# Kernel tuning notes

Measured on AMD Instinct MI355X. Metric: run time of the kernel, lower is better.

## Reference

```python
import jax, jax.numpy as jnp
import numpy as np

HEADS = 30
HEAD_DIM = 64
DIM = HEADS * HEAD_DIM  # 1920
TXT = 226
VID = 2048
EPS = 1e-5


def setup_inputs() -> dict:
    key = jax.random.key(0)
    ks = jax.random.split(key, 12)
    s = 1.0 / np.sqrt(DIM)
    return {
        "hidden_states": jax.random.normal(ks[0], (1, VID, DIM), jnp.float32),
        "encoder_hidden_states": jax.random.normal(ks[1], (1, TXT, DIM), jnp.float32),
        "rope_cos": jax.random.uniform(ks[2], (VID, HEAD_DIM), jnp.float32, -1.0, 1.0),
        "rope_sin": jax.random.uniform(ks[3], (VID, HEAD_DIM), jnp.float32, -1.0, 1.0),
        "Wq": jax.random.normal(ks[4], (DIM, DIM), jnp.float32) * s,
        "bq": jnp.zeros((DIM,), jnp.float32),
        "Wk": jax.random.normal(ks[5], (DIM, DIM), jnp.float32) * s,
        "bk": jnp.zeros((DIM,), jnp.float32),
        "Wv": jax.random.normal(ks[6], (DIM, DIM), jnp.float32) * s,
        "bv": jnp.zeros((DIM,), jnp.float32),
        "ln_q_w": jnp.ones((HEAD_DIM,), jnp.float32),
        "ln_q_b": jnp.zeros((HEAD_DIM,), jnp.float32),
        "ln_k_w": jnp.ones((HEAD_DIM,), jnp.float32),
        "ln_k_b": jnp.zeros((HEAD_DIM,), jnp.float32),
        "Wo": jax.random.normal(ks[7], (DIM, DIM), jnp.float32) * s,
        "bo": jnp.zeros((DIM,), jnp.float32),
    }


def _layernorm(x, w, b):
    mu = jnp.mean(x, axis=-1, keepdims=True)
    var = jnp.var(x, axis=-1, keepdims=True)
    return (x - mu) * jax.lax.rsqrt(var + EPS) * w + b


def _apply_rope(x, cos, sin):
    # x: [B,H,S_vid,D]; cos/sin: [S_vid,D]. Interleaved-pair rotation (diffusers use_real, unbind_dim=-1).
    xr = x[..., 0::2]
    xi = x[..., 1::2]
    rot = jnp.stack([-xi, xr], axis=-1).reshape(x.shape)
    return x * cos + rot * sin


def reference(hidden_states, encoder_hidden_states, rope_cos, rope_sin,
              Wq, bq, Wk, bk, Wv, bv, ln_q_w, ln_q_b, ln_k_w, ln_k_b, Wo, bo):
    T = encoder_hidden_states.shape[1]
    h = jnp.concatenate([encoder_hidden_states, hidden_states], axis=1)  # [B,S,D]
    B, S, _ = h.shape

    def proj(W, bias):
        y = h @ W.T + bias
        return y.reshape(B, S, HEADS, HEAD_DIM).transpose(0, 2, 1, 3)  # [B,H,S,d]

    q = proj(Wq, bq)
    k = proj(Wk, bk)
    v = proj(Wv, bv)

    q = _layernorm(q, ln_q_w, ln_q_b)
    k = _layernorm(k, ln_k_w, ln_k_b)

    # rotary embedding applied only to the image/video tokens
    q = jnp.concatenate([q[:, :, :T], _apply_rope(q[:, :, T:], rope_cos, rope_sin)], axis=2)
    k = jnp.concatenate([k[:, :, :T], _apply_rope(k[:, :, T:], rope_cos, rope_sin)], axis=2)

    scale = 1.0 / np.sqrt(HEAD_DIM)
    scores = jnp.einsum("bhqd,bhkd->bhqk", q, k) * scale
    attn = jax.nn.softmax(scores, axis=-1)
    out = jnp.einsum("bhqk,bhkd->bhqd", attn, v)

    out = out.transpose(0, 2, 1, 3).reshape(B, S, DIM)
    out = out @ Wo.T + bo
    return out[:, T:], out[:, :T]
```

## Files before the change

kernel.cpp:

```cpp
#include <hip/hip_runtime.h>
#include <hip/hip_bf16.h>

typedef __hip_bfloat16 bf16;
using f32x4 = __attribute__((ext_vector_type(4))) float;
using f32x16 = __attribute__((ext_vector_type(16))) float;
using s16x8 = __attribute__((ext_vector_type(8))) short;

#define S_TOT 2274
#define S_PAD 2304
#define TTXT 226
#define DIMN 1920
#define NH 30
#define HD 64
#define NQKV 5760
#define QSCALE 0.1803368801f

#define GLOAD_LDS16(g, l)                                                              \
  __builtin_amdgcn_global_load_lds((const __attribute__((address_space(1))) void*)(g), \
                                   (__attribute__((address_space(3))) void*)(l), 16, 0, 0)

__global__ void k_prep_h(const float* __restrict__ hid, const float* __restrict__ enc,
                         bf16* __restrict__ h_bf) {
  long i4 = ((long)blockIdx.x * blockDim.x + threadIdx.x) * 4;
  if (i4 >= (long)S_PAD * DIMN) return;
  int s = (int)(i4 / DIMN);
  float4 v = make_float4(0.f, 0.f, 0.f, 0.f);
  if (s < TTXT)
    v = *reinterpret_cast<const float4*>(enc + i4);
  else if (s < S_TOT)
    v = *reinterpret_cast<const float4*>(hid + i4 - (long)TTXT * DIMN);
  union {
    bf16 b[4];
    short4 s4;
  } o;
  o.b[0] = __float2bfloat16(v.x);
  o.b[1] = __float2bfloat16(v.y);
  o.b[2] = __float2bfloat16(v.z);
  o.b[3] = __float2bfloat16(v.w);
  *reinterpret_cast<short4*>(h_bf + i4) = o.s4;
}

__global__ void k_prep_wqkv(const float* __restrict__ Wq, const float* __restrict__ Wk,
                            const float* __restrict__ Wv, bf16* __restrict__ w_bf) {
  long i4 = ((long)blockIdx.x * blockDim.x + threadIdx.x) * 4;
  const long per = (long)DIMN * DIMN;
  if (i4 >= 3 * per) return;
  const float* src = (i4 < per) ? (Wq + i4) : (i4 < 2 * per) ? (Wk + i4 - per) : (Wv + i4 - 2 * per);
  float4 v = *reinterpret_cast<const float4*>(src);
  union {
    bf16 b[4];
    short4 s4;
  } o;
  o.b[0] = __float2bfloat16(v.x);
  o.b[1] = __float2bfloat16(v.y);
  o.b[2] = __float2bfloat16(v.z);
  o.b[3] = __float2bfloat16(v.w);
  *reinterpret_cast<short4*>(w_bf + i4) = o.s4;
}

__global__ void k_prep_wo(const float* __restrict__ Wo, bf16* __restrict__ w_bf) {
  long i4 = ((long)blockIdx.x * blockDim.x + threadIdx.x) * 4;
  if (i4 >= (long)DIMN * DIMN) return;
  float4 v = *reinterpret_cast<const float4*>(Wo + i4);
  union {
    bf16 b[4];
    short4 s4;
  } o;
  o.b[0] = __float2bfloat16(v.x);
  o.b[1] = __float2bfloat16(v.y);
  o.b[2] = __float2bfloat16(v.z);
  o.b[3] = __float2bfloat16(v.w);
  *reinterpret_cast<short4*>(w_bf + i4) = o.s4;
}

#define NKT 30
#define BUFSZ 49152
__global__ __launch_bounds__(512, 2) void k_gemm_qkv8(
    const bf16* __restrict__ A, const bf16* __restrict__ B, const float* __restrict__ bq,
    const float* __restrict__ bk, const float* __restrict__ bv, const float* __restrict__ lqw,
    const float* __restrict__ lqb, const float* __restrict__ lkw, const float* __restrict__ lkb,
    const float* __restrict__ cosT, const float* __restrict__ sinT, bf16* __restrict__ qb,
    bf16* __restrict__ kbf, bf16* __restrict__ vt) {
  __shared__ __align__(16) char smem[3 * BUFSZ];
  const int tid = threadIdx.x;
  const int w = tid >> 6, lane = tid & 63;
  const int clo = lane & 15, lhi = lane >> 4;
  const int wr = w >> 1, wc = w & 1;
  const int m0 = blockIdx.y * 256, n0 = blockIdx.x * 128;

  long ga[4], gb[2];
#pragma unroll
  for (int i = 0; i < 4; ++i) {
    const int s = i * 512 + tid;
    const int row = s >> 3, gch = (s & 7) ^ ((s >> 3) & 7);
    ga[i] = (long)(m0 + row) * DIMN + gch * 8;
  }
#pragma unroll
  for (int i = 0; i < 2; ++i) {
    const int s = i * 512 + tid;
    const int row = s >> 3, gch = (s & 7) ^ ((s >> 3) & 7);
    gb[i] = (long)(n0 + row) * DIMN + gch * 8;
  }
  const int wbase = w * 1024;

  auto stage = [&](int b, int kt) {
    char* Ab = &smem[b * BUFSZ];
    char* Bb = Ab + 32768;
    const int ko = kt * 64;
#pragma unroll
    for (int i = 0; i < 4; ++i) GLOAD_LDS16(A + ga[i] + ko, Ab + i * 8192 + wbase);
#pragma unroll
    for (int i = 0; i < 2; ++i) GLOAD_LDS16(B + gb[i] + ko, Bb + i * 8192 + wbase);
  };

  auto rdf = [&](const char* base, int row, int slot) {
    return *reinterpret_cast<const s16x8*>(base + row * 128 + ((slot ^ (row & 7)) * 16));
  };

  f32x4 acc[4][4] = {};

  stage(0, 0);
  stage(1, 1);
  for (int t = 0; t < NKT; ++t) {
    if (t < NKT - 1)
      asm volatile("s_waitcnt vmcnt(6)" ::: "memory");
    else
      asm volatile("s_waitcnt vmcnt(0)" ::: "memory");
    __builtin_amdgcn_s_barrier();
    if (t + 2 < NKT) stage((t + 2) % 3, t + 2);
    const char* Ab = &smem[(t % 3) * BUFSZ];
    const char* Bb = Ab + 32768;
#pragma unroll
    for (int ks = 0; ks < 2; ++ks) {
      s16x8 af[4], bfr[4];
#pragma unroll
      for (int m = 0; m < 4; ++m) af[m] = rdf(Ab, wr * 64 + m * 16 + clo, ks * 4 + lhi);
#pragma unroll
      for (int n = 0; n < 4; ++n) bfr[n] = rdf(Bb, wc * 64 + n * 16 + clo, ks * 4 + lhi);
      __builtin_amdgcn_s_setprio(1);
#pragma unroll
      for (int m = 0; m < 4; ++m)
#pragma unroll
        for (int n = 0; n < 4; ++n)
          acc[m][n] = __builtin_amdgcn_mfma_f32_16x16x32_bf16(af[m], bfr[n], acc[m][n], 0, 0, 0);
      __builtin_amdgcn_s_setprio(0);
    }
  }
  __syncthreads();

  const int gcol0 = n0 + wc * 64;
  const int sect = gcol0 / DIMN;
  const int hcol = gcol0 - sect * DIMN;
  const int head = hcol >> 6;
  const int row0 = m0 + wr * 64;

  if (sect < 2) {
    const float* bias = sect ? bk : bq;
    const float* lw = sect ? lkw : lqw;
    const float* lb = sect ? lkb : lqb;
    bf16* dst = sect ? kbf : qb;
    const float oscale = sect ? 1.f : QSCALE;
    float bb[4], lww[4], lbb[4];
#pragma unroll
    for (int n = 0; n < 4; ++n) {
      const int d = (n << 4) + clo;
      bb[n] = bias[hcol + d];
      lww[n] = lw[d];
      lbb[n] = lb[d];
    }
#pragma unroll
    for (int m = 0; m < 4; ++m) {
#pragma unroll
      for (int r = 0; r < 4; ++r) {
        const int row = row0 + m * 16 + lhi * 4 + r;
        float x[4];
#pragma unroll
        for (int n = 0; n < 4; ++n) x[n] = acc[m][n][r] + bb[n];
        float s_ = (x[0] + x[1]) + (x[2] + x[3]);
        float q_ = x[0] * x[0];
        q_ = fmaf(x[1], x[1], q_);
        q_ = fmaf(x[2], x[2], q_);
        q_ = fmaf(x[3], x[3], q_);
#pragma unroll
        for (int off = 1; off <= 8; off <<= 1) {
          s_ += __shfl_xor(s_, off);
          q_ += __shfl_xor(q_, off);
        }
        const float mu = s_ * (1.f / 64.f);
        const float var = q_ * (1.f / 64.f) - mu * mu;
        const float rst = rsqrtf(var + 1e-5f);
        float xn[4];
#pragma unroll
        for (int n = 0; n < 4; ++n) xn[n] = (x[n] - mu) * rst * lww[n] + lbb[n];
        const bool dorope = (row >= TTXT) && (row < S_TOT);
        if (dorope) {
          const float* cr = cosT + (long)(row - TTXT) * HD;
          const float* sr2 = sinT + (long)(row - TTXT) * HD;
#pragma unroll
          for (int n = 0; n < 4; ++n) {
            const int d = (n << 4) + clo;
            const float p = __shfl_xor(xn[n], 1);
            xn[n] = xn[n] * cr[d] + ((clo & 1) ? p : -p) * sr2[d];
          }
        }
#pragma unroll
        for (int n = 0; n < 4; ++n)
          dst[((long)head * S_PAD + row) * HD + (n << 4) + clo] =
              __float2bfloat16(xn[n] * oscale);
      }
    }
  } else {
    float bb[4];
#pragma unroll
    for (int n = 0; n < 4; ++n) bb[n] = bv[hcol + (n << 4) + clo];
    bf16* Lp = reinterpret_cast<bf16*>(smem + w * 9216);
#pragma unroll
    for (int m = 0; m < 4; ++m)
#pragma unroll
      for (int n = 0; n < 4; ++n)
#pragma unroll
        for (int r = 0; r < 4; ++r)
          Lp[((n << 4) + clo) * 72 + m * 16 + lhi * 4 + r] =
              __float2bfloat16(acc[m][n][r] + bb[n]);
    const int dsub = lane >> 3, sc = lane & 7;
#pragma unroll
    for (int it = 0; it < 8; ++it) {
      const int d = it * 8 + dsub;
      s16x8 v = *reinterpret_cast<const s16x8*>(&Lp[d * 72 + sc * 8]);
      *reinterpret_cast<s16x8*>(vt + ((long)head * HD + d) * S_PAD + row0 + sc * 8) = v;
    }
  }
}

__global__ __launch_bounds__(256) void k_gemm_proj(const bf16* __restrict__ A,
                                                   const bf16* __restrict__ B,
                                                   float* __restrict__ C,
                                                   const float* __restrict__ bias) {
  __shared__ __align__(16) char smem[32768];
  const int tid = threadIdx.x;
  const int w = tid >> 6, lane = tid & 63;
  const int clo = lane & 15, lhi = lane >> 4;
  const int wr = w >> 1, wc = w & 1;
  const int m0 = blockIdx.y * 128, n0 = blockIdx.x * 128;

  const int srow = tid >> 2, schunk = tid & 3;
  const long agoff0 = (long)(m0 + srow) * DIMN + schunk * 8;
  const long agoff1 = agoff0 + (long)64 * DIMN;
  const long bgoff0 = (long)(n0 + srow) * DIMN + schunk * 8;
  const long bgoff1 = bgoff0 + (long)64 * DIMN;
  const int ldsb = w * 1024;

  f32x4 acc[4][4] = {};

  auto stage = [&](int b, int kb) {
    char* Abuf = &smem[b * 16384];
    char* Bbuf = &smem[b * 16384 + 8192];
    GLOAD_LDS16(A + agoff0 + kb, Abuf + ldsb);
    GLOAD_LDS16(A + agoff1 + kb, Abuf + 4096 + ldsb);
    GLOAD_LDS16(B + bgoff0 + kb, Bbuf + ldsb);
    GLOAD_LDS16(B + bgoff1 + kb, Bbuf + 4096 + ldsb);
  };

  stage(0, 0);
  __syncthreads();
  int cur = 0;
  for (int ks = 0; ks < DIMN / 32; ++ks) {
    if (ks + 1 < DIMN / 32) stage(cur ^ 1, (ks + 1) * 32);
    const char* Abuf = &smem[cur * 16384];
    const char* Bbuf = &smem[cur * 16384 + 8192];
    s16x8 af[4], bfr[4];
#pragma unroll
    for (int m = 0; m < 4; ++m)
      af[m] = *reinterpret_cast<const s16x8*>(Abuf + (wr * 64 + m * 16 + clo) * 64 + lhi * 16);
#pragma unroll
    for (int n = 0; n < 4; ++n)
      bfr[n] = *reinterpret_cast<const s16x8*>(Bbuf + (wc * 64 + n * 16 + clo) * 64 + lhi * 16);
#pragma unroll
    for (int m = 0; m < 4; ++m)
#pragma unroll
      for (int n = 0; n < 4; ++n)
        acc[m][n] = __builtin_amdgcn_mfma_f32_16x16x32_bf16(af[m], bfr[n], acc[m][n], 0, 0, 0);
    __syncthreads();
    cur ^= 1;
  }
#pragma unroll
  for (int n = 0; n < 4; ++n) {
    const int col = n0 + wc * 64 + n * 16 + clo;
    const float bvv = bias[col];
#pragma unroll
    for (int m = 0; m < 4; ++m) {
#pragma unroll
      for (int r = 0; r < 4; ++r) {
        const int row = m0 + wr * 64 + m * 16 + lhi * 4 + r;
        if (row < S_TOT) {
          const int dst = (row >= TTXT) ? (row - TTXT) : (row + (S_TOT - TTXT));
          C[(long)dst * DIMN + col] = acc[m][n][r] + bvv;
        }
      }
    }
  }
}

__global__ __launch_bounds__(256) void k_flash6(const bf16* __restrict__ qb,
                                                const bf16* __restrict__ kbf,
                                                const bf16* __restrict__ vt,
                                                float* __restrict__ po,
                                                float* __restrict__ pm,
                                                float* __restrict__ pl) {
  __shared__ __align__(16) char smem[32768];
  const int h = blockIdx.x, qt = blockIdx.y, ks = blockIdx.z;
  const int tid = threadIdx.x, w = tid >> 6, lane = tid & 63;
  const int l31 = lane & 31, hf = lane >> 5;
  const bf16* Qh = qb + (long)h * S_PAD * HD;
  const bf16* Kh = kbf + (long)h * S_PAD * HD;
  const bf16* Vh = vt + (long)h * HD * S_PAD;
  const int q0w = qt * 128 + w * 32;
  const int T0 = ks * 18;

  s16x8 qf[4];
#pragma unroll
  for (int t = 0; t < 4; ++t)
    qf[t] = *reinterpret_cast<const s16x8*>(Qh + (long)(q0w + l31) * HD + t * 16 + hf * 8);

  f32x16 accO[2] = {};
  f32x16 lacc = {};
  float m_run = -1e30f;

  const s16x8 ones8 = {0x3F80, 0x3F80, 0x3F80, 0x3F80, 0x3F80, 0x3F80, 0x3F80, 0x3F80};

  const int su = w * 64 + lane;
  const int sr = su >> 3, sc8 = su & 7;
  const long kg0 = (long)sr * HD + ((sc8 ^ (sr & 7)) * 8);
  const long kg1 = kg0 + (long)32 * HD;
  const long vg0 = (long)sr * S_PAD + ((sc8 ^ (sr & 7)) * 8);
  const long vg1 = vg0 + (long)32 * S_PAD;
  const int ldsb = w * 1024;

  auto stage = [&](int b, int kb0) {
    char* Kb = &smem[b * 16384];
    char* Vb = &smem[b * 16384 + 8192];
    GLOAD_LDS16(Kh + (long)kb0 * HD + kg0, Kb + ldsb);
    GLOAD_LDS16(Kh + (long)kb0 * HD + kg1, Kb + 4096 + ldsb);
    GLOAD_LDS16(Vh + kb0 + vg0, Vb + ldsb);
    GLOAD_LDS16(Vh + kb0 + vg1, Vb + 4096 + ldsb);
  };

  auto ldsrd = [&](const char* base, int row, int c) {
    return *reinterpret_cast<const s16x8*>(base + row * 128 + ((c ^ (row & 7)) * 16));
  };
  auto pk2 = [&](float a, float b) -> unsigned {
    __hip_bfloat162 t = __float22bfloat162_rn(make_float2(a, b));
    return *reinterpret_cast<unsigned*>(&t);
  };

  stage(0, T0 * 64);
  __syncthreads();
  int cur = 0;
  for (int kt = 0; kt < 18; ++kt) {
    const int kb0 = (T0 + kt) * 64;
    if (kt + 1 < 18) stage(cur ^ 1, kb0 + 64);
    const char* Kb = &smem[cur * 16384];
    const char* Vb = &smem[cur * 16384 + 8192];

    f32x16 s0 = {}, s1 = {};
#pragma unroll
    for (int t = 0; t < 4; ++t) {
      s16x8 k0 = ldsrd(Kb, l31, 2 * t + hf);
      s16x8 k1 = ldsrd(Kb, 32 + l31, 2 * t + hf);
      s0 = __builtin_amdgcn_mfma_f32_32x32x16_bf16(k0, qf[t], s0, 0, 0, 0);
      s1 = __builtin_amdgcn_mfma_f32_32x32x16_bf16(k1, qf[t], s1, 0, 0, 0);
    }
    if (kb0 + 64 > S_TOT) {
#pragma unroll
      for (int j = 0; j < 16; ++j) {
        const int key = kb0 + (j & 3) + 8 * (j >> 2) + 4 * hf;
        if (key >= S_TOT) s0[j] = -1e30f;
        if (key + 32 >= S_TOT) s1[j] = -1e30f;
      }
    }
    float a8[8];
#pragma unroll
    for (int i = 0; i < 8; ++i)
      a8[i] = fmaxf(fmaxf(s0[2 * i], s0[2 * i + 1]), fmaxf(s1[2 * i], s1[2 * i + 1]));
    float pmax = fmaxf(fmaxf(fmaxf(a8[0], a8[1]), fmaxf(a8[2], a8[3])),
                       fmaxf(fmaxf(a8[4], a8[5]), fmaxf(a8[6], a8[7])));
    {
      auto r = __builtin_amdgcn_permlane32_swap(__float_as_uint(pmax), __float_as_uint(pmax),
                                                false, false);
      pmax = fmaxf(__uint_as_float(r[0]), __uint_as_float(r[1]));
    }
    if (!__all(pmax - m_run <= 8.f)) {
      const float mnew = fmaxf(m_run, pmax);
      const float corr = exp2f(m_run - mnew);
      m_run = mnew;
#pragma unroll
      for (int j = 0; j < 16; ++j) {
        const float cj = __shfl(corr, (lane & 32) | ((j & 3) + 8 * (j >> 2) + 4 * hf));
        accO[0][j] *= cj;
        accO[1][j] *= cj;
        lacc[j] *= cj;
      }
    }
#pragma unroll
    for (int j = 0; j < 16; ++j) {
      s0[j] = exp2f(s0[j] - m_run);
      s1[j] = exp2f(s1[j] - m_run);
    }
    unsigned gw0[8], gw1[8];
#pragma unroll
    for (int i = 0; i < 4; ++i) {
      gw0[2 * i] = pk2(s0[4 * i], s0[4 * i + 1]);
      gw0[2 * i + 1] = pk2(s0[4 * i + 2], s0[4 * i + 3]);
      gw1[2 * i] = pk2(s1[4 * i], s1[4 * i + 1]);
      gw1[2 * i + 1] = pk2(s1[4 * i + 2], s1[4 * i + 3]);
    }
    s16x8 pa[4];
#pragma unroll
    for (int b = 0; b < 2; ++b) {
      unsigned* gw = b ? gw1 : gw0;
#pragma unroll
      for (int t = 0; t < 2; ++t) {
        auto rA = __builtin_amdgcn_permlane32_swap(gw[4 * t + 0], gw[4 * t + 2], false, false);
        auto rB = __builtin_amdgcn_permlane32_swap(gw[4 * t + 1], gw[4 * t + 3], false, false);
        union {
          unsigned u[4];
          s16x8 v;
        } A;
        A.u[0] = rA[0];
        A.u[1] = rB[0];
        A.u[2] = rA[1];
        A.u[3] = rB[1];
        pa[b * 2 + t] = A.v;
      }
    }
#pragma unroll
    for (int t4 = 0; t4 < 4; ++t4) {
      s16x8 v0 = ldsrd(Vb, l31, 2 * t4 + hf);
      s16x8 v1 = ldsrd(Vb, 32 + l31, 2 * t4 + hf);
      accO[0] = __builtin_amdgcn_mfma_f32_32x32x16_bf16(pa[t4], v0, accO[0], 0, 0, 0);
      accO[1] = __builtin_amdgcn_mfma_f32_32x32x16_bf16(pa[t4], v1, accO[1], 0, 0, 0);
      lacc = __builtin_amdgcn_mfma_f32_32x32x16_bf16(pa[t4], ones8, lacc, 0, 0, 0);
    }
    __syncthreads();
    cur ^= 1;
  }
  const long rowbase = ((long)(ks * NH + h)) * S_PAD + q0w;
  if (hf == 0) pm[rowbase + l31] = m_run;
  if (l31 == 0) {
#pragma unroll
    for (int j = 0; j < 16; ++j) pl[rowbase + (j & 3) + 8 * (j >> 2) + 4 * hf] = lacc[j];
  }
#pragma unroll
  for (int j = 0; j < 16; ++j) {
    const int pat = (j & 3) + 8 * (j >> 2) + 4 * hf;
    float* dst = po + (rowbase + pat) * HD + l31;
    dst[0] = accO[0][j];
    dst[32] = accO[1][j];
  }
}

__global__ __launch_bounds__(256) void k_combine(const float* __restrict__ po,
                                                 const float* __restrict__ pm,
                                                 const float* __restrict__ pl,
                                                 bf16* __restrict__ ao) {
  const int idx = blockIdx.x * 256 + threadIdx.x;
  const int d = idx & 63;
  const int row = (idx >> 6) % S_PAD;
  const int h = idx / (S_PAD * 64);
  if (row >= S_TOT) return;
  const long r1 = (long)h * S_PAD + row;
  const long r2 = (long)(NH + h) * S_PAD + row;
  const float m1 = pm[r1], m2 = pm[r2];
  const float m = fmaxf(m1, m2);
  const float a1 = exp2f(m1 - m), a2 = exp2f(m2 - m);
  const float o = po[r1 * HD + d] * a1 + po[r2 * HD + d] * a2;
  const float l = pl[r1] * a1 + pl[r2] * a2;
  ao[(long)row * DIMN + h * HD + d] = __float2bfloat16(o / l);
}

extern "C" void kernel_launch(void* const* d_in, const int* in_sizes, int n_in, void* d_out,
                              int out_size, void* d_ws, size_t ws_size, hipStream_t stream) {
  const float* hid = (const float*)d_in[0];
  const float* enc = (const float*)d_in[1];
  const float* rc = (const float*)d_in[2];
  const float* rs = (const float*)d_in[3];
  const float* Wq = (const float*)d_in[4];
  const float* bq = (const float*)d_in[5];
  const float* Wk = (const float*)d_in[6];
  const float* bk = (const float*)d_in[7];
  const float* Wv = (const float*)d_in[8];
  const float* bv = (const float*)d_in[9];
  const float* lqw = (const float*)d_in[10];
  const float* lqb = (const float*)d_in[11];
  const float* lkw = (const float*)d_in[12];
  const float* lkb = (const float*)d_in[13];
  const float* Wo = (const float*)d_in[14];
  const float* bo = (const float*)d_in[15];
  float* out = (float*)d_out;

  char* ws = (char*)d_ws;
  size_t off = 0;
  char* scratch = ws + off;
  off += (size_t)S_PAD * NQKV * 4;
  bf16* h_bf = (bf16*)(ws + off);
  off += (size_t)S_PAD * DIMN * 2;
  bf16* wqkv = (bf16*)(ws + off);
  off += (size_t)3 * DIMN * DIMN * 2;
  bf16* wo = (bf16*)(ws + off);
  off += (size_t)DIMN * DIMN * 2;
  bf16* q_bf = (bf16*)(ws + off);
  off += (size_t)NH * S_PAD * HD * 2;
  bf16* k_bf = (bf16*)(ws + off);
  off += (size_t)NH * S_PAD * HD * 2;
  bf16* vt_bf = (bf16*)(ws + off);
  off += (size_t)NH * HD * S_PAD * 2;
  bf16* at_bf = (bf16*)(ws + off);
  off += (size_t)S_PAD * DIMN * 2;

  float* po = (float*)scratch;
  float* pm = (float*)(scratch + (size_t)2 * NH * S_PAD * HD * 4);
  float* pl = pm + (size_t)2 * NH * S_PAD;

  k_prep_h<<<((S_PAD * DIMN) / 4 + 255) / 256, 256, 0, stream>>>(hid, enc, h_bf);
  k_prep_wqkv<<<((3 * DIMN * DIMN) / 4 + 255) / 256, 256, 0, stream>>>(Wq, Wk, Wv, wqkv);
  k_prep_wo<<<((DIMN * DIMN) / 4 + 255) / 256, 256, 0, stream>>>(Wo, wo);
  k_gemm_qkv8<<<dim3(NQKV / 128, S_PAD / 256), 512, 0, stream>>>(
      h_bf, wqkv, bq, bk, bv, lqw, lqb, lkw, lkb, rc, rs, q_bf, k_bf, vt_bf);
  k_flash6<<<dim3(NH, S_PAD / 128, 2), 256, 0, stream>>>(q_bf, k_bf, vt_bf, po, pm, pl);
  k_combine<<<NH * S_PAD * HD / 256, 256, 0, stream>>>(po, pm, pl, at_bf);
  k_gemm_proj<<<dim3(DIMN / 128, S_PAD / 128), 256, 0, stream>>>(at_bf, wo, out, bo);
}
```

Baseline: 254.7 us.

## Retile QKV, flash and output-projection kernels for higher occupancy and deeper pipelining

The QKV GEMM moves from a 64-wide K step to a 32-wide one, with smaller triple-buffered LDS stages so four blocks can share a CU. The flash attention kernel goes from 256 to 512 threads, with 256 queries per block sharing each staged K/V tile. The output projection GEMM now uses 8 waves with a triple-buffered 64-wide K pipeline, replacing the 4-wave double-buffered loop that synchronised every step. Together these aim to raise occupancy and overlap loads with compute, at the cost of more barriers in the QKV kernel and more register pressure.

```diff
diff --git a/kernel.cpp b/kernel.cpp
--- a/kernel.cpp
+++ b/kernel.cpp
@@ -73,78 +73,65 @@
   *reinterpret_cast<short4*>(w_bf + i4) = o.s4;
 }
 
-#define NKT 30
-#define BUFSZ 49152
-__global__ __launch_bounds__(512, 2) void k_gemm_qkv8(
+#define NKT32 60
+#define QBUF 24576
+__global__ __launch_bounds__(512, 4) void k_gemm_qkv9(
     const bf16* __restrict__ A, const bf16* __restrict__ B, const float* __restrict__ bq,
     const float* __restrict__ bk, const float* __restrict__ bv, const float* __restrict__ lqw,
     const float* __restrict__ lqb, const float* __restrict__ lkw, const float* __restrict__ lkb,
     const float* __restrict__ cosT, const float* __restrict__ sinT, bf16* __restrict__ qb,
     bf16* __restrict__ kbf, bf16* __restrict__ vt) {
-  __shared__ __align__(16) char smem[3 * BUFSZ];
+  __shared__ __align__(16) char smem[3 * QBUF];
   const int tid = threadIdx.x;
   const int w = tid >> 6, lane = tid & 63;
   const int clo = lane & 15, lhi = lane >> 4;
   const int wr = w >> 1, wc = w & 1;
   const int m0 = blockIdx.y * 256, n0 = blockIdx.x * 128;
 
-  long ga[4], gb[2];
-#pragma unroll
-  for (int i = 0; i < 4; ++i) {
-    const int s = i * 512 + tid;
-    const int row = s >> 3, gch = (s & 7) ^ ((s >> 3) & 7);
-    ga[i] = (long)(m0 + row) * DIMN + gch * 8;
-  }
-#pragma unroll
-  for (int i = 0; i < 2; ++i) {
-    const int s = i * 512 + tid;
-    const int row = s >> 3, gch = (s & 7) ^ ((s >> 3) & 7);
-    gb[i] = (long)(n0 + row) * DIMN + gch * 8;
-  }
+  const int u1 = 512 + tid;
+  const long ga0 = (long)(m0 + (tid >> 2)) * DIMN + (((tid & 3) ^ ((tid >> 2) & 3)) * 8);
+  const long ga1 = (long)(m0 + (u1 >> 2)) * DIMN + (((u1 & 3) ^ ((u1 >> 2) & 3)) * 8);
+  const long gb0 = (long)(n0 + (tid >> 2)) * DIMN + (((tid & 3) ^ ((tid >> 2) & 3)) * 8);
   const int wbase = w * 1024;
 
   auto stage = [&](int b, int kt) {
-    char* Ab = &smem[b * BUFSZ];
-    char* Bb = Ab + 32768;
-    const int ko = kt * 64;
-#pragma unroll
-    for (int i = 0; i < 4; ++i) GLOAD_LDS16(A + ga[i] + ko, Ab + i * 8192 + wbase);
-#pragma unroll
-    for (int i = 0; i < 2; ++i) GLOAD_LDS16(B + gb[i] + ko, Bb + i * 8192 + wbase);
-  };
-
-  auto rdf = [&](const char* base, int row, int slot) {
-    return *reinterpret_cast<const s16x8*>(base + row * 128 + ((slot ^ (row & 7)) * 16));
+    char* Ab = &smem[b * QBUF];
+    char* Bb = Ab + 16384;
+    const int ko = kt * 32;
+    GLOAD_LDS16(A + ga0 + ko, Ab + wbase);
+    GLOAD_LDS16(A + ga1 + ko, Ab + 8192 + wbase);
+    GLOAD_LDS16(B + gb0 + ko, Bb + wbase);
+  };
+
+  auto rdf = [&](const char* base, int row) {
+    return *reinterpret_cast<const s16x8*>(base + row * 64 + ((lhi ^ (row & 3)) * 16));
   };
 
   f32x4 acc[4][4] = {};
 
   stage(0, 0);
   stage(1, 1);
-  for (int t = 0; t < NKT; ++t) {
-    if (t < NKT - 1)
-      asm volatile("s_waitcnt vmcnt(6)" ::: "memory");
+  for (int t = 0; t < NKT32; ++t) {
+    if (t < NKT32 - 1)
+      asm volatile("s_waitcnt vmcnt(3)" ::: "memory");
     else
       asm volatile("s_waitcnt vmcnt(0)" ::: "memory");
     __builtin_amdgcn_s_barrier();
-    if (t + 2 < NKT) stage((t + 2) % 3, t + 2);
-    const char* Ab = &smem[(t % 3) * BUFSZ];
-    const char* Bb = Ab + 32768;
-#pragma unroll
-    for (int ks = 0; ks < 2; ++ks) {
-      s16x8 af[4], bfr[4];
-#pragma unroll
-      for (int m = 0; m < 4; ++m) af[m] = rdf(Ab, wr * 64 + m * 16 + clo, ks * 4 + lhi);
-#pragma unroll
-      for (int n = 0; n < 4; ++n) bfr[n] = rdf(Bb, wc * 64 + n * 16 + clo, ks * 4 + lhi);
-      __builtin_amdgcn_s_setprio(1);
-#pragma unroll
-      for (int m = 0; m < 4; ++m)
-#pragma unroll
-        for (int n = 0; n < 4; ++n)
-          acc[m][n] = __builtin_amdgcn_mfma_f32_16x16x32_bf16(af[m], bfr[n], acc[m][n], 0, 0, 0);
-      __builtin_amdgcn_s_setprio(0);
-    }
+    if (t + 2 < NKT32) stage((t + 2) % 3, t + 2);
+    const char* Ab = &smem[(t % 3) * QBUF];
+    const char* Bb = Ab + 16384;
+    s16x8 af[4], bfr[4];
+#pragma unroll
+    for (int m = 0; m < 4; ++m) af[m] = rdf(Ab, wr * 64 + m * 16 + clo);
+#pragma unroll
+    for (int n = 0; n < 4; ++n) bfr[n] = rdf(Bb, wc * 64 + n * 16 + clo);
+    __builtin_amdgcn_s_setprio(1);
+#pragma unroll
+    for (int m = 0; m < 4; ++m)
+#pragma unroll
+      for (int n = 0; n < 4; ++n)
+        acc[m][n] = __builtin_amdgcn_mfma_f32_16x16x32_bf16(af[m], bfr[n], acc[m][n], 0, 0, 0);
+    __builtin_amdgcn_s_setprio(0);
   }
   __syncthreads();
 
@@ -232,60 +219,76 @@
   }
 }
 
-__global__ __launch_bounds__(256) void k_gemm_proj(const bf16* __restrict__ A,
-                                                   const bf16* __restrict__ B,
-                                                   float* __restrict__ C,
-                                                   const float* __restrict__ bias) {
-  __shared__ __align__(16) char smem[32768];
+#define NKT 30
+#define PBUF 32768
+__global__ __launch_bounds__(512, 2) void k_gemm_proj8(const bf16* __restrict__ A,
+                                                       const bf16* __restrict__ B,
+                                                       float* __restrict__ C,
+                                                       const float* __restrict__ bias) {
+  __shared__ __align__(16) char smem[3 * PBUF];
   const int tid = threadIdx.x;
   const int w = tid >> 6, lane = tid & 63;
   const int clo = lane & 15, lhi = lane >> 4;
-  const int wr = w >> 1, wc = w & 1;
+  const int wr = w >> 2, wc = w & 3;
   const int m0 = blockIdx.y * 128, n0 = blockIdx.x * 128;
 
-  const int srow = tid >> 2, schunk = tid & 3;
-  const long agoff0 = (long)(m0 + srow) * DIMN + schunk * 8;
-  const long agoff1 = agoff0 + (long)64 * DIMN;
-  const long bgoff0 = (long)(n0 + srow) * DIMN + schunk * 8;
-  const long bgoff1 = bgoff0 + (long)64 * DIMN;
-  const int ldsb = w * 1024;
-
-  f32x4 acc[4][4] = {};
-
-  auto stage = [&](int b, int kb) {
-    char* Abuf = &smem[b * 16384];
-    char* Bbuf = &smem[b * 16384 + 8192];
-    GLOAD_LDS16(A + agoff0 + kb, Abuf + ldsb);
-    GLOAD_LDS16(A + agoff1 + kb, Abuf + 4096 + ldsb);
-    GLOAD_LDS16(B + bgoff0 + kb, Bbuf + ldsb);
-    GLOAD_LDS16(B + bgoff1 + kb, Bbuf + 4096 + ldsb);
-  };
+  long ga[2], gb[2];
+#pragma unroll
+  for (int i = 0; i < 2; ++i) {
+    const int s = i * 512 + tid;
+    const int row = s >> 3, gch = (s & 7) ^ ((s >> 3) & 7);
+    ga[i] = (long)(m0 + row) * DIMN + gch * 8;
+    gb[i] = (long)(n0 + row) * DIMN + gch * 8;
+  }
+  const int wbase = w * 1024;
+
+  auto stage = [&](int b, int kt) {
+    char* Ab = &smem[b * PBUF];
+    char* Bb = Ab + 16384;
+    const int ko = kt * 64;
+#pragma unroll
+    for (int i = 0; i < 2; ++i) {
+      GLOAD_LDS16(A + ga[i] + ko, Ab + i * 8192 + wbase);
+      GLOAD_LDS16(B + gb[i] + ko, Bb + i * 8192 + wbase);
+    }
+  };
+
+  auto rdf = [&](const char* base, int row, int slot) {
+    return *reinterpret_cast<const s16x8*>(base + row * 128 + ((slot ^ (row & 7)) * 16));
+  };
+
+  f32x4 acc[4][2] = {};
 
   stage(0, 0);
-  __syncthreads();
-  int cur = 0;
-  for (int ks = 0; ks < DIMN / 32; ++ks) {
-    if (ks + 1 < DIMN / 32) stage(cur ^ 1, (ks + 1) * 32);
-    const char* Abuf = &smem[cur * 16384];
-    const char* Bbuf = &smem[cur * 16384 + 8192];
-    s16x8 af[4], bfr[4];
-#pragma unroll
-    for (int m = 0; m < 4; ++m)
-      af[m] = *reinterpret_cast<const s16x8*>(Abuf + (wr * 64 + m * 16 + clo) * 64 + lhi * 16);
-#pragma unroll
-    for (int n = 0; n < 4; ++n)
-      bfr[n] = *reinterpret_cast<const s16x8*>(Bbuf + (wc * 64 + n * 16 + clo) * 64 + lhi * 16);
-#pragma unroll
-    for (int m = 0; m < 4; ++m)
-#pragma unroll
-      for (int n = 0; n < 4; ++n)
-        acc[m][n] = __builtin_amdgcn_mfma_f32_16x16x32_bf16(af[m], bfr[n], acc[m][n], 0, 0, 0);
-    __syncthreads();
-    cur ^= 1;
-  }
-#pragma unroll
-  for (int n = 0; n < 4; ++n) {
-    const int col = n0 + wc * 64 + n * 16 + clo;
+  stage(1, 1);
+  for (int t = 0; t < NKT; ++t) {
+    if (t < NKT - 1)
+      asm volatile("s_waitcnt vmcnt(4)" ::: "memory");
+    else
+      asm volatile("s_waitcnt vmcnt(0)" ::: "memory");
+    __builtin_amdgcn_s_barrier();
+    if (t + 2 < NKT) stage((t + 2) % 3, t + 2);
+    const char* Ab = &smem[(t % 3) * PBUF];
+    const char* Bb = Ab + 16384;
+#pragma unroll
+    for (int ks = 0; ks < 2; ++ks) {
+      s16x8 af[4], bfr[2];
+#pragma unroll
+      for (int m = 0; m < 4; ++m) af[m] = rdf(Ab, wr * 64 + m * 16 + clo, ks * 4 + lhi);
+#pragma unroll
+      for (int n = 0; n < 2; ++n) bfr[n] = rdf(Bb, wc * 32 + n * 16 + clo, ks * 4 + lhi);
+      __builtin_amdgcn_s_setprio(1);
+#pragma unroll
+      for (int m = 0; m < 4; ++m)
+#pragma unroll
+        for (int n = 0; n < 2; ++n)
+          acc[m][n] = __builtin_amdgcn_mfma_f32_16x16x32_bf16(af[m], bfr[n], acc[m][n], 0, 0, 0);
+      __builtin_amdgcn_s_setprio(0);
+    }
+  }
+#pragma unroll
+  for (int n = 0; n < 2; ++n) {
+    const int col = n0 + wc * 32 + n * 16 + clo;
     const float bvv = bias[col];
 #pragma unroll
     for (int m = 0; m < 4; ++m) {
@@ -301,12 +304,12 @@
   }
 }
 
-__global__ __launch_bounds__(256) void k_flash6(const bf16* __restrict__ qb,
-                                                const bf16* __restrict__ kbf,
-                                                const bf16* __restrict__ vt,
-                                                float* __restrict__ po,
-                                                float* __restrict__ pm,
-                                                float* __restrict__ pl) {
+__global__ __launch_bounds__(512, 4) void k_flash9(const bf16* __restrict__ qb,
+                                                   const bf16* __restrict__ kbf,
+                                                   const bf16* __restrict__ vt,
+                                                   float* __restrict__ po,
+                                                   float* __restrict__ pm,
+                                                   float* __restrict__ pl) {
   __shared__ __align__(16) char smem[32768];
   const int h = blockIdx.x, qt = blockIdx.y, ks = blockIdx.z;
   const int tid = threadIdx.x, w = tid >> 6, lane = tid & 63;
@@ -314,7 +317,7 @@
   const bf16* Qh = qb + (long)h * S_PAD * HD;
   const bf16* Kh = kbf + (long)h * S_PAD * HD;
   const bf16* Vh = vt + (long)h * HD * S_PAD;
-  const int q0w = qt * 128 + w * 32;
+  const int q0w = qt * 256 + w * 32;
   const int T0 = ks * 18;
 
   s16x8 qf[4];
@@ -328,21 +331,16 @@
 
   const s16x8 ones8 = {0x3F80, 0x3F80, 0x3F80, 0x3F80, 0x3F80, 0x3F80, 0x3F80, 0x3F80};
 
-  const int su = w * 64 + lane;
-  const int sr = su >> 3, sc8 = su & 7;
+  const int sr = tid >> 3, sc8 = tid & 7;
   const long kg0 = (long)sr * HD + ((sc8 ^ (sr & 7)) * 8);
-  const long kg1 = kg0 + (long)32 * HD;
   const long vg0 = (long)sr * S_PAD + ((sc8 ^ (sr & 7)) * 8);
-  const long vg1 = vg0 + (long)32 * S_PAD;
   const int ldsb = w * 1024;
 
   auto stage = [&](int b, int kb0) {
     char* Kb = &smem[b * 16384];
     char* Vb = &smem[b * 16384 + 8192];
     GLOAD_LDS16(Kh + (long)kb0 * HD + kg0, Kb + ldsb);
-    GLOAD_LDS16(Kh + (long)kb0 * HD + kg1, Kb + 4096 + ldsb);
     GLOAD_LDS16(Vh + kb0 + vg0, Vb + ldsb);
-    GLOAD_LDS16(Vh + kb0 + vg1, Vb + 4096 + ldsb);
   };
 
   auto ldsrd = [&](const char* base, int row, int c) {
@@ -524,9 +522,9 @@
   k_prep_h<<<((S_PAD * DIMN) / 4 + 255) / 256, 256, 0, stream>>>(hid, enc, h_bf);
   k_prep_wqkv<<<((3 * DIMN * DIMN) / 4 + 255) / 256, 256, 0, stream>>>(Wq, Wk, Wv, wqkv);
   k_prep_wo<<<((DIMN * DIMN) / 4 + 255) / 256, 256, 0, stream>>>(Wo, wo);
-  k_gemm_qkv8<<<dim3(NQKV / 128, S_PAD / 256), 512, 0, stream>>>(
+  k_gemm_qkv9<<<dim3(NQKV / 128, S_PAD / 256), 512, 0, stream>>>(
       h_bf, wqkv, bq, bk, bv, lqw, lqb, lkw, lkb, rc, rs, q_bf, k_bf, vt_bf);
-  k_flash6<<<dim3(NH, S_PAD / 128, 2), 256, 0, stream>>>(q_bf, k_bf, vt_bf, po, pm, pl);
+  k_flash9<<<dim3(NH, S_PAD / 256, 2), 512, 0, stream>>>(q_bf, k_bf, vt_bf, po, pm, pl);
   k_combine<<<NH * S_PAD * HD / 256, 256, 0, stream>>>(po, pm, pl, at_bf);
-  k_gemm_proj<<<dim3(DIMN / 128, S_PAD / 128), 256, 0, stream>>>(at_bf, wo, out, bo);
-}
+  k_gemm_proj8<<<dim3(DIMN / 128, S_PAD / 128), 512, 0, stream>>>(at_bf, wo, out, bo);
+}
```

Result: faster. 245.9 us (-3.4%).
